# Kernel tuning notes

Measured on AMD Instinct MI355X. Metric: run time of the kernel, lower is better.

## Reference

```python
import jax, jax.numpy as jnp
import numpy as np
import math

H = 16  # n_head
DK = 64  # d_k = n_feat // n_head
BASE = 10000.0


def _rope_cos_sin(T, dk, dtype):
    inv_freq = 1.0 / (BASE ** (jnp.arange(0, dk, 2, dtype=jnp.float32) / dk))
    t = jnp.arange(T, dtype=jnp.float32)
    freqs = jnp.einsum('i,j->ij', t, inv_freq)          # [T, dk/2]
    emb = jnp.concatenate([freqs, freqs], axis=-1)       # [T, dk]
    return jnp.cos(emb).astype(dtype)[:, None, None, :], jnp.sin(emb).astype(dtype)[:, None, None, :]


def _rotate_half(x):
    x1, x2 = jnp.split(x, 2, axis=-1)
    return jnp.concatenate([-x2, x1], axis=-1)


def setup_inputs() -> dict:
    key = jax.random.key(0)
    ks = jax.random.split(key, 8)
    T, B, C = 2048, 2, 1024
    s = 0.02
    return {
        'query': jax.random.normal(ks[0], (T, B, C), jnp.float32),
        'key': jax.random.normal(ks[1], (T, B, C), jnp.float32),
        'value': jax.random.normal(ks[2], (T, B, C), jnp.float32),
        'Wq': jax.random.normal(ks[3], (C, C), jnp.float32) * s,
        'bq': jnp.zeros((C,), jnp.float32),
        'Wk': jax.random.normal(ks[4], (C, C), jnp.float32) * s,
        'bk': jnp.zeros((C,), jnp.float32),
        'Wv': jax.random.normal(ks[5], (C, C), jnp.float32) * s,
        'bv': jnp.zeros((C,), jnp.float32),
        'Wo': jax.random.normal(ks[6], (C, C), jnp.float32) * s,
        'bo': jnp.zeros((C,), jnp.float32),
    }


def reference(query, key, value, Wq, bq, Wk, bk, Wv, bv, Wo, bo):
    T, B, C = value.shape
    # --- RoPE applied to raw inputs (per the original module), before projections ---
    q = query.reshape(T, B, H, DK)
    k = key.reshape(T, B, H, DK)
    cos, sin = _rope_cos_sin(T, DK, q.dtype)  # [T,1,1,DK]
    q = q * cos + _rotate_half(q) * sin
    k = k * cos + _rotate_half(k) * sin
    q = q.reshape(T, B, C).transpose(1, 0, 2)   # [B,T,C]
    k = k.reshape(T, B, C).transpose(1, 0, 2)
    v = value.transpose(1, 0, 2)
    # --- QKV projections (torch Linear: x @ W.T + b) ---
    q = (jnp.einsum('btc,dc->btd', q, Wq) + bq).reshape(B, T, H, DK).transpose(0, 2, 1, 3)
    k = (jnp.einsum('btc,dc->btd', k, Wk) + bk).reshape(B, T, H, DK).transpose(0, 2, 1, 3)
    v = (jnp.einsum('btc,dc->btd', v, Wv) + bv).reshape(B, T, H, DK).transpose(0, 2, 1, 3)
    # --- scaled dot-product attention ---
    scores = jnp.einsum('bhqd,bhkd->bhqk', q, k) / math.sqrt(DK)
    attn = jax.nn.softmax(scores, axis=-1)
    x = jnp.einsum('bhqk,bhkd->bhqd', attn, v)        # [B,H,T,DK]
    x = x.transpose(0, 2, 1, 3).reshape(B, T, C)
    out = jnp.einsum('btc,dc->btd', x, Wo) + bo        # [B,T,C]
    return out.transpose(1, 0, 2)                      # [T,B,C]
```

## Files before the change

kernel.cpp:

```cpp
#include <hip/hip_runtime.h>
#include <hip/hip_bf16.h>
#include <math.h>

#define T_SEQ 2048
#define B_SZ 2
#define C_DIM 1024
#define H_HEADS 16
#define DKH 64
#define M_ROWS (T_SEQ * B_SZ)

#define QSCALE 0.1803368801111204f

typedef __attribute__((ext_vector_type(8))) short bf16x8;
typedef __attribute__((ext_vector_type(4))) float f32x4;
typedef unsigned short ushort_t;


__device__ __forceinline__ ushort_t f2bf(float f) {
    unsigned u = __float_as_uint(f);
    u += 0x7fffu + ((u >> 16) & 1u);
    return (ushort_t)(u >> 16);
}

__device__ __forceinline__ unsigned pack2bf(float a, float b) {
#if __has_builtin(__builtin_amdgcn_cvt_pk_bf16_f32)
    typedef __attribute__((ext_vector_type(2))) __bf16 bf16x2_t;
    union { bf16x2_t v; unsigned u; } cv;
    cv.v = __builtin_amdgcn_cvt_pk_bf16_f32(a, b);
    return cv.u;
#else
    return (unsigned)f2bf(a) | ((unsigned)f2bf(b) << 16);
#endif
}

__device__ __forceinline__ void async_copy16(const void* g, void* l) {
    __builtin_amdgcn_global_load_lds(
        (const __attribute__((address_space(1))) void*)g,
        (__attribute__((address_space(3))) void*)l, 16, 0, 0);
}

__global__ __launch_bounds__(256) void rope_cast_qk(
        const float* __restrict__ q, const float* __restrict__ k,
        ushort_t* __restrict__ qb, ushort_t* __restrict__ kb) {
    int idx  = blockIdx.x * 256 + threadIdx.x;
    int j    = idx & 31;
    int rest = idx >> 5;
    int h    = rest & (H_HEADS - 1);
    int tb   = rest >> 4;
    int t    = tb >> 1;
    float inv = exp2f(-(float)j * 0.41524101186092034f);
    float ang = (float)t * inv;
    float s, c;
    sincosf(ang, &s, &c);
    int base = tb * C_DIM + h * DKH + j;
    float q1 = q[base], q2 = q[base + 32];
    float k1 = k[base], k2 = k[base + 32];
    qb[base]      = f2bf(q1 * c - q2 * s);
    qb[base + 32] = f2bf(q2 * c + q1 * s);
    kb[base]      = f2bf(k1 * c - k2 * s);
    kb[base + 32] = f2bf(k2 * c + k1 * s);
}

__global__ __launch_bounds__(256) void cast_bf16(
        const float* __restrict__ in, ushort_t* __restrict__ out, int n4) {
    int i = blockIdx.x * 256 + threadIdx.x;
    if (i < n4) {
        float4 v = reinterpret_cast<const float4*>(in)[i];
        ushort4 o;
        o.x = f2bf(v.x); o.y = f2bf(v.y); o.z = f2bf(v.z); o.w = f2bf(v.w);
        reinterpret_cast<ushort4*>(out)[i] = o;
    }
}

__global__ __launch_bounds__(256) void cast_value_perm(
        const float* __restrict__ in, ushort_t* __restrict__ out) {
    int i   = blockIdx.x * 256 + threadIdx.x;
    int c4  = i & 255;
    int row = i >> 8;
    int b   = row >> 11, t = row & 2047;
    float4 v = reinterpret_cast<const float4*>(in)[(t * 2 + b) * 256 + c4];
    ushort4 o;
    o.x = f2bf(v.x); o.y = f2bf(v.y); o.z = f2bf(v.z); o.w = f2bf(v.w);
    reinterpret_cast<ushort4*>(out)[i] = o;
}

template <bool BF16_OUT, bool BIAS_ROW>
__global__ __launch_bounds__(512) void gemm_nt(
        const ushort_t* __restrict__ A, const ushort_t* __restrict__ W,
        const float* __restrict__ bias, void* __restrict__ Cout,
        int M, int N, int K, float scale) {
    __shared__ ushort_t As[128 * 64];
    __shared__ ushort_t Bs[64 * 64];
    const int tid  = threadIdx.x;
    const int lane = tid & 63;
    const int w    = tid >> 6;
    const int m16  = lane & 15, quad = lane >> 4;
    const int r8   = lane >> 3, c8 = lane & 7;
    const int clog = c8 ^ r8;
    const int rowBase = blockIdx.y * 128;
    const int colBase = blockIdx.x * 64;

    f32x4 acc[4];
#pragma unroll
    for (int j = 0; j < 4; j++) acc[j] = (f32x4){0.f, 0.f, 0.f, 0.f};

    for (int kt = 0; kt < K; kt += 64) {
        __syncthreads();
#pragma unroll
        for (int i = 0; i < 2; ++i) {
            int R = w * 16 + i * 8;
            async_copy16(A + (size_t)(rowBase + R + r8) * K + kt + clog * 8,
                         &As[R * 64]);
        }
        {
            int R = w * 8;
            async_copy16(W + (size_t)(colBase + R + r8) * K + kt + clog * 8,
                         &Bs[R * 64]);
        }
        __syncthreads();
#pragma unroll
        for (int ks = 0; ks < 2; ++ks) {
            int lc = ks * 4 + quad;
            bf16x8 af;
            {
                int R = w * 16 + m16;
                af = *reinterpret_cast<const bf16x8*>(
                    &As[R * 64 + ((lc ^ (R & 7)) << 3)]);
            }
            bf16x8 bfr[4];
#pragma unroll
            for (int ni = 0; ni < 4; ni++) {
                int R = ni * 16 + m16;
                bfr[ni] = *reinterpret_cast<const bf16x8*>(
                    &Bs[R * 64 + ((lc ^ (R & 7)) << 3)]);
            }
#pragma unroll
            for (int ni = 0; ni < 4; ni++)
                acc[ni] = __builtin_amdgcn_mfma_f32_16x16x32_bf16(
                    af, bfr[ni], acc[ni], 0, 0, 0);
        }
    }
#pragma unroll
    for (int ni = 0; ni < 4; ni++)
#pragma unroll
        for (int r = 0; r < 4; r++) {
            int row = rowBase + w * 16 + quad * 4 + r;
            int col = colBase + ni * 16 + m16;
            float v = (acc[ni][r] + (BIAS_ROW ? bias[row] : bias[col])) * scale;
            if (BF16_OUT)
                ((ushort_t*)Cout)[(size_t)row * N + col] = f2bf(v);
            else
                ((float*)Cout)[(size_t)row * N + col] = v;
        }
}

__global__ __launch_bounds__(256) void attn(
        const ushort_t* __restrict__ Qp, const ushort_t* __restrict__ Kp,
        const ushort_t* __restrict__ VTg, ushort_t* __restrict__ X) {
    __shared__ char smem[40960];
    ushort_t* Qt = (ushort_t*)smem;
    char*  KtC   = smem + 8192;
    char*  VTC   = smem + 24576;
    float* exch  = (float*)(smem + 8192);
    float* lbuf  = (float*)smem;

    const int tid  = threadIdx.x;
    const int lane = tid & 63;
    const int w    = tid >> 6;
    const int m16  = lane & 15, quad = lane >> 4;
    const int r8   = lane >> 3, c8 = lane & 7;
    const int clog = c8 ^ r8;

    const int lid   = blockIdx.x + blockIdx.y * 32;
    const int jj    = lid >> 3;
    const int pair  = (lid & 7) * 4 + (jj >> 5);
    const int qBase = (jj & 31) * 64;
    const int b = pair >> 4, h = pair & 15;

    const int ofA = m16 * 128 + ((quad ^ (m16 & 7)) << 4);
    const int ofB = m16 * 128 + (((4 + quad) ^ (m16 & 7)) << 4);
    const int fro = m16 * 64 + ((quad ^ (m16 & 3)) << 4);
    int pw0[2];
#pragma unroll
    for (int kt_i = 0; kt_i < 2; kt_i++)
        pw0[kt_i] = m16 * 64 + ((((kt_i * 2 + (quad >> 1)) ^ (m16 & 3))) << 4) + (quad & 1) * 8;
    char* PwC = KtC + w * 4096;

#pragma unroll
    for (int i = 0; i < 2; ++i) {
        int R = w * 16 + i * 8;
        async_copy16(Qp + (size_t)((qBase + R + r8) * 2 + b) * C_DIM + h * DKH + clog * 8,
                     &Qt[R * 64]);
    }
    __syncthreads();
    bf16x8 aq[4][2];
#pragma unroll
    for (int ni = 0; ni < 4; ni++) {
        aq[ni][0] = *reinterpret_cast<const bf16x8*>((const char*)Qt + ni * 2048 + ofA);
        aq[ni][1] = *reinterpret_cast<const bf16x8*>((const char*)Qt + ni * 2048 + ofB);
    }
    asm volatile("s_waitcnt lgkmcnt(0)" ::: "memory");
    __syncthreads();

    float lrun[4] = {0.f, 0.f, 0.f, 0.f};
    f32x4 o[4][4];
#pragma unroll
    for (int mi = 0; mi < 4; mi++)
#pragma unroll
        for (int ni = 0; ni < 4; ni++) o[mi][ni] = (f32x4){0.f, 0.f, 0.f, 0.f};

    for (int kt = 0; kt < T_SEQ; kt += 128) {
        asm volatile("s_waitcnt lgkmcnt(0)" ::: "memory");
#pragma unroll
        for (int i = 0; i < 4; ++i) {
            int key = kt + w * 32 + i * 8 + r8;
            async_copy16(Kp + (size_t)(key * 2 + b) * C_DIM + h * DKH + clog * 8,
                         KtC + w * 4096 + i * 1024);
        }
#pragma unroll
        for (int i = 0; i < 4; ++i) {
            int dkr = i * 16 + (lane >> 2);
            int lc  = (lane & 3) ^ ((lane >> 2) & 3);
            async_copy16(VTg + (size_t)(h * DKH + dkr) * M_ROWS + b * T_SEQ + kt + w * 32 + lc * 8,
                         VTC + w * 4096 + i * 1024);
        }
        asm volatile("s_waitcnt vmcnt(0)" ::: "memory");
        __builtin_amdgcn_sched_barrier(0);

        f32x4 s[2][4];
#pragma unroll
        for (int kt_i = 0; kt_i < 2; kt_i++) {
#pragma unroll
            for (int ni = 0; ni < 4; ni++) s[kt_i][ni] = (f32x4){0.f, 0.f, 0.f, 0.f};
            bf16x8 kf0 = *reinterpret_cast<const bf16x8*>(KtC + w * 4096 + kt_i * 2048 + ofA);
            bf16x8 kf1 = *reinterpret_cast<const bf16x8*>(KtC + w * 4096 + kt_i * 2048 + ofB);
#pragma unroll
            for (int ni = 0; ni < 4; ni++) {
                s[kt_i][ni] = __builtin_amdgcn_mfma_f32_16x16x32_bf16(kf0, aq[ni][0], s[kt_i][ni], 0, 0, 0);
                s[kt_i][ni] = __builtin_amdgcn_mfma_f32_16x16x32_bf16(kf1, aq[ni][1], s[kt_i][ni], 0, 0, 0);
            }
        }

#pragma unroll
        for (int kt_i = 0; kt_i < 2; kt_i++)
#pragma unroll
            for (int ni = 0; ni < 4; ni++) {
                float p0 = __builtin_amdgcn_exp2f(s[kt_i][ni][0]);
                float p1 = __builtin_amdgcn_exp2f(s[kt_i][ni][1]);
                float p2 = __builtin_amdgcn_exp2f(s[kt_i][ni][2]);
                float p3 = __builtin_amdgcn_exp2f(s[kt_i][ni][3]);
                lrun[ni] += (p0 + p1) + (p2 + p3);
                uint2 pv;
                pv.x = pack2bf(p0, p1);
                pv.y = pack2bf(p2, p3);
                *reinterpret_cast<uint2*>(PwC + ni * 1024 + pw0[kt_i]) = pv;
            }
        asm volatile("s_waitcnt lgkmcnt(0)" ::: "memory");

        bf16x8 pf[4];
#pragma unroll
        for (int ni = 0; ni < 4; ni++)
            pf[ni] = *reinterpret_cast<const bf16x8*>(PwC + ni * 1024 + fro);
#pragma unroll
        for (int mi = 0; mi < 4; mi++) {
            bf16x8 vf = *reinterpret_cast<const bf16x8*>(VTC + w * 4096 + mi * 1024 + fro);
#pragma unroll
            for (int ni = 0; ni < 4; ni++)
                o[mi][ni] = __builtin_amdgcn_mfma_f32_16x16x32_bf16(vf, pf[ni], o[mi][ni], 0, 0, 0);
        }
    }

#pragma unroll
    for (int ni = 0; ni < 4; ni++) {
        lrun[ni] += __shfl_xor(lrun[ni], 16);
        lrun[ni] += __shfl_xor(lrun[ni], 32);
    }
    float lv = quad == 0 ? lrun[0] : quad == 1 ? lrun[1] : quad == 2 ? lrun[2] : lrun[3];
    lbuf[w * 64 + quad * 16 + m16] = lv;

    __syncthreads();

#pragma unroll
    for (int rnd = 0; rnd < 2; rnd++) {
        if (rnd) __syncthreads();
#pragma unroll
        for (int t2 = 0; t2 < 2; t2++) {
            int mi = 2 * rnd + t2;
#pragma unroll
            for (int ni = 0; ni < 4; ni++) {
                int q = ni * 16 + m16;
                int cw = t2 * 4 + quad;
                *reinterpret_cast<f32x4*>(
                    &exch[w * 2048 + q * 32 + ((cw ^ (q & 7)) << 2)]) = o[mi][ni];
            }
        }
        __syncthreads();
        int q = tid >> 2;
        float lsum = lbuf[q] + lbuf[64 + q] + lbuf[128 + q] + lbuf[192 + q];
        float invl = 1.0f / lsum;
#pragma unroll
        for (int half = 0; half < 2; half++) {
            int c = (tid & 3) + 4 * half;
            int off = q * 32 + (((c ^ (q & 7))) << 2);
            f32x4 v = *reinterpret_cast<const f32x4*>(&exch[off]);
            f32x4 v1 = *reinterpret_cast<const f32x4*>(&exch[2048 + off]);
            f32x4 v2 = *reinterpret_cast<const f32x4*>(&exch[4096 + off]);
            f32x4 v3 = *reinterpret_cast<const f32x4*>(&exch[6144 + off]);
            v = v + v1 + v2 + v3;
            uint2 pk;
            pk.x = pack2bf(v[0] * invl, v[1] * invl);
            pk.y = pack2bf(v[2] * invl, v[3] * invl);
            int t = qBase + q;
            *reinterpret_cast<uint2*>(
                &X[(size_t)(t * 2 + b) * C_DIM + h * DKH + rnd * 32 + c * 4]) = pk;
        }
    }
}

extern "C" void kernel_launch(void* const* d_in, const int* in_sizes, int n_in,
                              void* d_out, int out_size, void* d_ws, size_t ws_size,
                              hipStream_t stream) {
    const float* query = (const float*)d_in[0];
    const float* key   = (const float*)d_in[1];
    const float* value = (const float*)d_in[2];
    const float* Wq = (const float*)d_in[3];
    const float* bq = (const float*)d_in[4];
    const float* Wk = (const float*)d_in[5];
    const float* bk = (const float*)d_in[6];
    const float* Wv = (const float*)d_in[7];
    const float* bv = (const float*)d_in[8];
    const float* Wo = (const float*)d_in[9];
    const float* bo = (const float*)d_in[10];
    float* out = (float*)d_out;

    ushort_t* qb  = (ushort_t*)d_ws;
    ushort_t* kb  = qb  + (size_t)M_ROWS * C_DIM;
    ushort_t* vb2 = kb  + (size_t)M_ROWS * C_DIM;
    ushort_t* Wqb = vb2 + (size_t)M_ROWS * C_DIM;
    ushort_t* Wkb = Wqb + (size_t)C_DIM * C_DIM;
    ushort_t* Wvb = Wkb + (size_t)C_DIM * C_DIM;
    ushort_t* Wob = Wvb + (size_t)C_DIM * C_DIM;
    ushort_t* Qp  = Wob + (size_t)C_DIM * C_DIM;
    ushort_t* Kp  = Qp  + (size_t)M_ROWS * C_DIM;
    ushort_t* VTg = Kp  + (size_t)M_ROWS * C_DIM;
    ushort_t* Xb  = VTg + (size_t)M_ROWS * C_DIM;

    rope_cast_qk<<<(T_SEQ * B_SZ * H_HEADS * 32) / 256, 256, 0, stream>>>(query, key, qb, kb);
    cast_value_perm<<<(M_ROWS * C_DIM / 4) / 256, 256, 0, stream>>>(value, vb2);
    cast_bf16<<<(C_DIM * C_DIM / 4) / 256, 256, 0, stream>>>(Wq, Wqb, C_DIM * C_DIM / 4);
    cast_bf16<<<(C_DIM * C_DIM / 4) / 256, 256, 0, stream>>>(Wk, Wkb, C_DIM * C_DIM / 4);
    cast_bf16<<<(C_DIM * C_DIM / 4) / 256, 256, 0, stream>>>(Wv, Wvb, C_DIM * C_DIM / 4);
    cast_bf16<<<(C_DIM * C_DIM / 4) / 256, 256, 0, stream>>>(Wo, Wob, C_DIM * C_DIM / 4);

    dim3 gg(C_DIM / 64, M_ROWS / 128);
    gemm_nt<true, false><<<gg, 512, 0, stream>>>(qb, Wqb, bq, Qp, M_ROWS, C_DIM, C_DIM, QSCALE);
    gemm_nt<true, false><<<gg, 512, 0, stream>>>(kb, Wkb, bk, Kp, M_ROWS, C_DIM, C_DIM, 1.0f);
    dim3 gv(M_ROWS / 64, C_DIM / 128);
    gemm_nt<true, true><<<gv, 512, 0, stream>>>(Wvb, vb2, bv, VTg, C_DIM, M_ROWS, C_DIM, 1.0f);

    attn<<<dim3(T_SEQ / 64, B_SZ * H_HEADS), 256, 0, stream>>>(Qp, Kp, VTg, Xb);

    gemm_nt<false, false><<<gg, 512, 0, stream>>>(Xb, Wob, bo, (void*)out, M_ROWS, C_DIM, C_DIM, 1.0f);
}
```

Before: 255.8 us.

## Prefetch next K/V tile during PV MFMAs and merge weight casts

The attention loop now issues the async global-to-LDS copies for the next K/V tile right after the current P and V fragments are loaded into registers, so those loads overlap the PV matrix multiplies. The P/V LDS swizzle is changed to a different bank pattern, and the kernel gets an occupancy hint of four blocks. The four separate weight-cast launches are merged into one 2D launch to cut launch overhead. The risks are register pressure from holding V fragments and the occupancy bound, plus buffer aliasing between P and K.

```diff
diff --git a/kernel.cpp b/kernel.cpp
--- a/kernel.cpp
+++ b/kernel.cpp
@@ -61,15 +61,19 @@
     kb[base + 32] = f2bf(k2 * c + k1 * s);
 }
 
-__global__ __launch_bounds__(256) void cast_bf16(
-        const float* __restrict__ in, ushort_t* __restrict__ out, int n4) {
+__global__ __launch_bounds__(256) void cast_bf16_w4(
+        const float* __restrict__ w0, const float* __restrict__ w1,
+        const float* __restrict__ w2, const float* __restrict__ w3,
+        ushort_t* __restrict__ o0, ushort_t* __restrict__ o1,
+        ushort_t* __restrict__ o2, ushort_t* __restrict__ o3) {
+    int which = blockIdx.y;
+    const float* in = which == 0 ? w0 : which == 1 ? w1 : which == 2 ? w2 : w3;
+    ushort_t*   out = which == 0 ? o0 : which == 1 ? o1 : which == 2 ? o2 : o3;
     int i = blockIdx.x * 256 + threadIdx.x;
-    if (i < n4) {
-        float4 v = reinterpret_cast<const float4*>(in)[i];
-        ushort4 o;
-        o.x = f2bf(v.x); o.y = f2bf(v.y); o.z = f2bf(v.z); o.w = f2bf(v.w);
-        reinterpret_cast<ushort4*>(out)[i] = o;
-    }
+    float4 v = reinterpret_cast<const float4*>(in)[i];
+    ushort4 o;
+    o.x = f2bf(v.x); o.y = f2bf(v.y); o.z = f2bf(v.z); o.w = f2bf(v.w);
+    reinterpret_cast<ushort4*>(out)[i] = o;
 }
 
 __global__ __launch_bounds__(256) void cast_value_perm(
@@ -154,7 +158,7 @@
         }
 }
 
-__global__ __launch_bounds__(256) void attn(
+__global__ __launch_bounds__(256, 4) void attn(
         const ushort_t* __restrict__ Qp, const ushort_t* __restrict__ Kp,
         const ushort_t* __restrict__ VTg, ushort_t* __restrict__ X) {
     __shared__ char smem[40960];
@@ -179,12 +183,15 @@
 
     const int ofA = m16 * 128 + ((quad ^ (m16 & 7)) << 4);
     const int ofB = m16 * 128 + (((4 + quad) ^ (m16 & 7)) << 4);
-    const int fro = m16 * 64 + ((quad ^ (m16 & 3)) << 4);
+    const int sw4 = (m16 >> 1) & 3;
+    const int fro = m16 * 64 + ((quad ^ sw4) << 4);
     int pw0[2];
 #pragma unroll
     for (int kt_i = 0; kt_i < 2; kt_i++)
-        pw0[kt_i] = m16 * 64 + ((((kt_i * 2 + (quad >> 1)) ^ (m16 & 3))) << 4) + (quad & 1) * 8;
+        pw0[kt_i] = m16 * 64 + (((kt_i * 2 + (quad >> 1)) ^ sw4) << 4) + (quad & 1) * 8;
     char* PwC = KtC + w * 4096;
+
+    const int vlc = (lane & 3) ^ ((lane >> 3) & 3);
 
 #pragma unroll
     for (int i = 0; i < 2; ++i) {
@@ -209,8 +216,7 @@
 #pragma unroll
         for (int ni = 0; ni < 4; ni++) o[mi][ni] = (f32x4){0.f, 0.f, 0.f, 0.f};
 
-    for (int kt = 0; kt < T_SEQ; kt += 128) {
-        asm volatile("s_waitcnt lgkmcnt(0)" ::: "memory");
+    auto stageKV = [&](int kt) {
 #pragma unroll
         for (int i = 0; i < 4; ++i) {
             int key = kt + w * 32 + i * 8 + r8;
@@ -220,10 +226,13 @@
 #pragma unroll
         for (int i = 0; i < 4; ++i) {
             int dkr = i * 16 + (lane >> 2);
-            int lc  = (lane & 3) ^ ((lane >> 2) & 3);
-            async_copy16(VTg + (size_t)(h * DKH + dkr) * M_ROWS + b * T_SEQ + kt + w * 32 + lc * 8,
+            async_copy16(VTg + (size_t)(h * DKH + dkr) * M_ROWS + b * T_SEQ + kt + w * 32 + vlc * 8,
                          VTC + w * 4096 + i * 1024);
         }
+    };
+
+    stageKV(0);
+    for (int kt = 0; kt < T_SEQ; kt += 128) {
         asm volatile("s_waitcnt vmcnt(0)" ::: "memory");
         __builtin_amdgcn_sched_barrier(0);
 
@@ -261,13 +270,20 @@
 #pragma unroll
         for (int ni = 0; ni < 4; ni++)
             pf[ni] = *reinterpret_cast<const bf16x8*>(PwC + ni * 1024 + fro);
-#pragma unroll
-        for (int mi = 0; mi < 4; mi++) {
-            bf16x8 vf = *reinterpret_cast<const bf16x8*>(VTC + w * 4096 + mi * 1024 + fro);
+        bf16x8 vfr[4];
+#pragma unroll
+        for (int mi = 0; mi < 4; mi++)
+            vfr[mi] = *reinterpret_cast<const bf16x8*>(VTC + w * 4096 + mi * 1024 + fro);
+        asm volatile("s_waitcnt lgkmcnt(0)" ::: "memory");
+        __builtin_amdgcn_sched_barrier(0);
+        if (kt + 128 < T_SEQ) stageKV(kt + 128);
+        __builtin_amdgcn_sched_barrier(0);
+
+#pragma unroll
+        for (int mi = 0; mi < 4; mi++)
 #pragma unroll
             for (int ni = 0; ni < 4; ni++)
-                o[mi][ni] = __builtin_amdgcn_mfma_f32_16x16x32_bf16(vf, pf[ni], o[mi][ni], 0, 0, 0);
-        }
+                o[mi][ni] = __builtin_amdgcn_mfma_f32_16x16x32_bf16(vfr[mi], pf[ni], o[mi][ni], 0, 0, 0);
     }
 
 #pragma unroll
@@ -347,10 +363,8 @@
 
     rope_cast_qk<<<(T_SEQ * B_SZ * H_HEADS * 32) / 256, 256, 0, stream>>>(query, key, qb, kb);
     cast_value_perm<<<(M_ROWS * C_DIM / 4) / 256, 256, 0, stream>>>(value, vb2);
-    cast_bf16<<<(C_DIM * C_DIM / 4) / 256, 256, 0, stream>>>(Wq, Wqb, C_DIM * C_DIM / 4);
-    cast_bf16<<<(C_DIM * C_DIM / 4) / 256, 256, 0, stream>>>(Wk, Wkb, C_DIM * C_DIM / 4);
-    cast_bf16<<<(C_DIM * C_DIM / 4) / 256, 256, 0, stream>>>(Wv, Wvb, C_DIM * C_DIM / 4);
-    cast_bf16<<<(C_DIM * C_DIM / 4) / 256, 256, 0, stream>>>(Wo, Wob, C_DIM * C_DIM / 4);
+    dim3 cg((C_DIM * C_DIM / 4) / 256, 4);
+    cast_bf16_w4<<<cg, 256, 0, stream>>>(Wq, Wk, Wv, Wo, Wqb, Wkb, Wvb, Wob);
 
     dim3 gg(C_DIM / 64, M_ROWS / 128);
     gemm_nt<true, false><<<gg, 512, 0, stream>>>(qb, Wqb, bq, Qp, M_ROWS, C_DIM, C_DIM, QSCALE);
```

Result: slower. 441.8 us (+72.7%).
